# Kernel optimization log

Hardware: AMD Instinct MI355X
Metric: run time of the kernel (lower is better)

Reference implementation:

```python
import jax, jax.numpy as jnp
import numpy as np

B, T, D_IN, D_OUT, N_FILT, MAX_T = 4, 2048, 512, 512, 24, 2048


def _hankel_filters(max_t: int, k: int) -> np.ndarray:
    # Z_{ij} = 2 / ((i+j)^3 - (i+j)), 1-indexed; top-|eig| eigenvectors
    idx = np.arange(1, max_t + 1, dtype=np.float64)
    ij = idx[None, :] + idx[:, None]
    Z = 2.0 / (ij ** 3 - ij)
    w, v = np.linalg.eigh(Z)
    top = np.argsort(-np.abs(w))[:k]
    return v[:, top].astype(np.float32)  # (max_t, k)


def setup_inputs() -> dict:
    key = jax.random.key(0)
    kx, km = jax.random.split(key)
    x = jax.random.normal(kx, (B, T, D_IN), dtype=jnp.float32)
    filters = jnp.asarray(_hankel_filters(MAX_T, N_FILT))  # (MAX_T, N)
    # nn.Linear weight is (d_out, d_in); stacked -> (N, d_out, d_in)
    scale = 1.0 / np.sqrt(D_IN)
    M_weights = jax.random.uniform(km, (N_FILT, D_OUT, D_IN), dtype=jnp.float32,
                                   minval=-scale, maxval=scale)
    return {"x": x, "filters": filters, "M_weights": M_weights}


def reference(x, filters, M_weights):
    Tlen = x.shape[1]
    phi = filters[:Tlen]                       # (T, N)
    phi_e = phi[None, :, :, None]              # (1, T, N, 1)
    weighted = phi_e * x[:, :, None, :]        # (B, T, N, D_in)
    csum = jnp.cumsum(weighted, axis=1)        # causal cumulative projection
    # per-filter rectangular projection: (B,T,N,f) x (N,o,f) -> (B,T,N,o)
    modulated = jnp.einsum('btnf,nof->btno', csum, M_weights)
    return (phi_e * modulated).sum(axis=2)     # (B, T, D_out)
```

## Files before the change

kernel.cpp:

```cpp
#include <hip/hip_runtime.h>
#include <stdint.h>

#define BQ 4
#define TT 2048
#define DF 512
#define DOUT 512
#define NF 24
#define CHF 8

typedef __attribute__((ext_vector_type(8))) short short8;
typedef __attribute__((ext_vector_type(4))) float f32x4;

typedef __attribute__((address_space(3))) uint8_t       lds_u8;
typedef __attribute__((address_space(1))) const uint8_t glb_u8;

__device__ __forceinline__ float bf2f(unsigned short u) {
    union { unsigned int i; float f; } v; v.i = ((unsigned int)u) << 16; return v.f;
}
__device__ __forceinline__ unsigned short f2bf(float f) {
    union { float f; unsigned int i; } v; v.f = f;
    unsigned int r = v.i + 0x7FFFu + ((v.i >> 16) & 1u);
    return (unsigned short)(r >> 16);
}
__device__ __forceinline__ float lo16f(unsigned int u) { return __uint_as_float(u << 16); }
__device__ __forceinline__ float hi16f(unsigned int u) { return __uint_as_float(u & 0xffff0000u); }

__device__ __forceinline__ int plaus16(unsigned int h) {
    unsigned int e = (h >> 7) & 0xffu;
    return (e >= 97u && e <= 141u) || ((h & 0x7fffu) == 0u);
}

__global__ void k_detect(const unsigned int* __restrict__ X, int* __restrict__ flag)
{
    const int lane = threadIdx.x;
    int cnt = 0;
#pragma unroll
    for (int i = 0; i < 4; ++i) {
        unsigned int w = X[lane * 4 + i];
        cnt += (plaus16(w >> 16) && plaus16(w & 0xffffu)) ? 1 : 0;
    }
    for (int off = 32; off > 0; off >>= 1) cnt += __shfl_down(cnt, off);
    if (lane == 0) *flag = (cnt < 180) ? 1 : 0;
}

__global__ __launch_bounds__(256) void k_convert(
    const void* __restrict__ src, unsigned short* __restrict__ dst,
    const int* __restrict__ flag, int n4)
{
    const int isf32 = *flag;
    int i = blockIdx.x * 256 + threadIdx.x;
    const int stride = gridDim.x * 256;
    for (; i < n4; i += stride) {
        ushort4 o;
        if (isf32) {
            float4 v = ((const float4*)src)[i];
            o.x = f2bf(v.x); o.y = f2bf(v.y); o.z = f2bf(v.z); o.w = f2bf(v.w);
        } else {
            o = ((const ushort4*)src)[i];
        }
        ((ushort4*)dst)[i] = o;
    }
}

__global__ __launch_bounds__(256) void k_convf(
    const void* __restrict__ src, float* __restrict__ dst,
    const int* __restrict__ flag, int n)
{
    const int isf32 = *flag;
    int i = blockIdx.x * 256 + threadIdx.x;
    const int stride = gridDim.x * 256;
    for (; i < n; i += stride)
        dst[i] = isf32 ? ((const float*)src)[i]
                       : bf2f(((const unsigned short*)src)[i]);
}

__global__ __launch_bounds__(256, 3) void k_gemm_fast(
    const unsigned short* __restrict__ X,
    const unsigned short* __restrict__ Mw,
    const float* __restrict__ Fw,
    unsigned short* __restrict__ Z,
    float* __restrict__ Cs,
    int r0)
{
    __shared__ unsigned short sAB[128 * 136];
    __shared__ float sPhi[128];
    unsigned short* const sC = sAB;

    const int tid  = threadIdx.x;
    const int lane = tid & 63;
    const int w    = tid >> 6;
    const int wm   = w & 1, wn = w >> 1;
    const int tm   = blockIdx.x;
    const int on0  = blockIdx.y * 128;
    const int n    = blockIdx.z;

    const int rowg0 = r0 + tm * 128;
    if (tid < 128)
        sPhi[tid] = Fw[((rowg0 + tid) & (TT - 1)) * NF + n];

    const unsigned short* Ag = X + (size_t)rowg0 * DF;
    const unsigned short* Bg = Mw + (size_t)n * DOUT * DF + (size_t)on0 * DF;

    auto stage = [&](int kt, int buf) {
        const unsigned short* Ak = Ag + kt * 32;
        const unsigned short* Bk = Bg + kt * 32;
        lds_u8* base = (lds_u8*)sAB + buf * 16384;
#pragma unroll
        for (int i = 0; i < 2; ++i) {
            const int cbase = i * 256 + w * 64;
            const int c = cbase + lane;
            const int r = c >> 2, qs = c & 3;
            const int qg = qs ^ ((r >> 1) & 3);
            __builtin_amdgcn_global_load_lds(
                (const glb_u8*)(Ak + (size_t)r * DF + qg * 8),
                base + cbase * 16, 16, 0, 0);
            __builtin_amdgcn_global_load_lds(
                (const glb_u8*)(Bk + (size_t)r * DF + qg * 8),
                base + 8192 + cbase * 16, 16, 0, 0);
        }
    };

    f32x4 acc[4][4];
#pragma unroll
    for (int i = 0; i < 4; i++)
#pragma unroll
        for (int j = 0; j < 4; j++) acc[i][j] = (f32x4){0.f, 0.f, 0.f, 0.f};

    stage(0, 0);
    __syncthreads();

    const int lr = lane & 15;
    const int q  = lane >> 4;
    const int qsw = (q ^ ((lr >> 1) & 3)) * 8;

    for (int kt = 0; kt < DF / 32; ++kt) {
        const int cur = kt & 1;
        if (kt < DF / 32 - 1) stage(kt + 1, cur ^ 1);

        const unsigned short* sAc = sAB + cur * 8192;
        const unsigned short* sBc = sAc + 4096;
        short8 a[4], b[4];
#pragma unroll
        for (int i = 0; i < 4; i++)
            a[i] = *(const short8*)&sAc[(wm * 64 + i * 16 + lr) * 32 + qsw];
#pragma unroll
        for (int j = 0; j < 4; j++)
            b[j] = *(const short8*)&sBc[(wn * 64 + j * 16 + lr) * 32 + qsw];
#pragma unroll
        for (int i = 0; i < 4; i++)
#pragma unroll
            for (int j = 0; j < 4; j++)
                acc[i][j] = __builtin_amdgcn_mfma_f32_16x16x32_bf16(
                    a[i], b[j], acc[i][j], 0, 0, 0);

        __syncthreads();
    }

    const int rb = (lane >> 4) * 4;
#pragma unroll
    for (int i = 0; i < 4; i++)
#pragma unroll
        for (int j = 0; j < 4; j++)
#pragma unroll
            for (int r = 0; r < 4; r++) {
                int row = wm * 64 + i * 16 + rb + r;
                sC[row * 136 + wn * 64 + j * 16 + (lane & 15)] =
                    f2bf(acc[i][j][r] * sPhi[row]);
            }
    __syncthreads();

#pragma unroll
    for (int it = 0; it < 8; ++it) {
        int row = it * 16 + (tid >> 4);
        int col = (tid & 15) * 8;
        uint4 v = *(const uint4*)&sC[row * 136 + col];
        *(uint4*)&Z[((size_t)(tm * 128 + row) * NF + n) * 512 + on0 + col] = v;
    }

    {
        const int ci  = tid >> 4;
        const int col = (tid & 15) * 8;
        float s0=0.f,s1=0.f,s2=0.f,s3=0.f,s4=0.f,s5=0.f,s6=0.f,s7=0.f;
#pragma unroll
        for (int r = 0; r < CHF; ++r) {
            uint4 v = *(const uint4*)&sC[(ci * CHF + r) * 136 + col];
            s0 += lo16f(v.x); s1 += hi16f(v.x);
            s2 += lo16f(v.y); s3 += hi16f(v.y);
            s4 += lo16f(v.z); s5 += hi16f(v.z);
            s6 += lo16f(v.w); s7 += hi16f(v.w);
        }
        float* cp = &Cs[((size_t)(tm * 16 + ci) * NF + n) * 512 + on0 + col];
        *(float4*)cp       = make_float4(s0, s1, s2, s3);
        *(float4*)(cp + 4) = make_float4(s4, s5, s6, s7);
    }
}

__global__ __launch_bounds__(256, 2) void k_gemm(
    const void* __restrict__ Xv, const void* __restrict__ Mv,
    const void* __restrict__ Fv, const int* __restrict__ flag,
    unsigned short* __restrict__ Z, int r0, int o0, int W)
{
    __shared__ unsigned short sA[128 * 32];
    __shared__ unsigned short sB[128 * 32];
    __shared__ unsigned short sC[128 * 136];
    __shared__ float sPhi[128];

    const int isf32 = *flag;
    const int tid  = threadIdx.x;
    const int lane = tid & 63;
    const int w    = tid >> 6;
    const int wm   = w & 1, wn = w >> 1;
    const int tm   = blockIdx.x;
    const int on0  = o0 + blockIdx.y * 128;
    const int n    = blockIdx.z;

    const int rowg0 = r0 + tm * 128;
    if (tid < 128) {
        int t = (rowg0 + tid) & (TT - 1);
        sPhi[tid] = isf32 ? ((const float*)Fv)[t * NF + n]
                          : bf2f(((const unsigned short*)Fv)[t * NF + n]);
    }

    const unsigned short* Ah = (const unsigned short*)Xv + (size_t)rowg0 * DF;
    const unsigned short* Bh = (const unsigned short*)Mv +
        (size_t)n * DOUT * DF + (size_t)on0 * DF;
    const float* Af = (const float*)Xv + (size_t)rowg0 * DF;
    const float* Bf = (const float*)Mv + (size_t)n * DOUT * DF + (size_t)on0 * DF;

    f32x4 acc[4][4];
#pragma unroll
    for (int i = 0; i < 4; i++)
#pragma unroll
        for (int j = 0; j < 4; j++) acc[i][j] = (f32x4){0.f, 0.f, 0.f, 0.f};

    for (int kt = 0; kt < DF / 32; ++kt) {
        __syncthreads();
        if (!isf32) {
            const unsigned short* Ak = Ah + kt * 32;
            const unsigned short* Bk = Bh + kt * 32;
#pragma unroll
            for (int i = 0; i < 2; ++i) {
                const int c = i * 256 + tid;
                const int r = c >> 2, cc = (c & 3) * 8;
                *(short8*)&sA[r * 32 + cc] = *(const short8*)(Ak + (size_t)r * DF + cc);
                *(short8*)&sB[r * 32 + cc] = *(const short8*)(Bk + (size_t)r * DF + cc);
            }
        } else {
            const float* Ak = Af + kt * 32;
            const float* Bk = Bf + kt * 32;
#pragma unroll
            for (int i = 0; i < 2; ++i) {
                const int c = i * 256 + tid;
                const int r = c >> 2, cc = (c & 3) * 8;
                float4 a0 = *(const float4*)(Ak + (size_t)r * DF + cc);
                float4 a1 = *(const float4*)(Ak + (size_t)r * DF + cc + 4);
                float4 b0 = *(const float4*)(Bk + (size_t)r * DF + cc);
                float4 b1 = *(const float4*)(Bk + (size_t)r * DF + cc + 4);
                short8 sa, sb;
                sa[0]=(short)f2bf(a0.x); sa[1]=(short)f2bf(a0.y);
                sa[2]=(short)f2bf(a0.z); sa[3]=(short)f2bf(a0.w);
                sa[4]=(short)f2bf(a1.x); sa[5]=(short)f2bf(a1.y);
                sa[6]=(short)f2bf(a1.z); sa[7]=(short)f2bf(a1.w);
                sb[0]=(short)f2bf(b0.x); sb[1]=(short)f2bf(b0.y);
                sb[2]=(short)f2bf(b0.z); sb[3]=(short)f2bf(b0.w);
                sb[4]=(short)f2bf(b1.x); sb[5]=(short)f2bf(b1.y);
                sb[6]=(short)f2bf(b1.z); sb[7]=(short)f2bf(b1.w);
                *(short8*)&sA[r * 32 + cc] = sa;
                *(short8*)&sB[r * 32 + cc] = sb;
            }
        }
        __syncthreads();

        const int lr = lane & 15;
        const int lk = (lane >> 4) * 8;
        short8 a[4], b[4];
#pragma unroll
        for (int i = 0; i < 4; i++)
            a[i] = *(const short8*)&sA[(wm * 64 + i * 16 + lr) * 32 + lk];
#pragma unroll
        for (int j = 0; j < 4; j++)
            b[j] = *(const short8*)&sB[(wn * 64 + j * 16 + lr) * 32 + lk];
#pragma unroll
        for (int i = 0; i < 4; i++)
#pragma unroll
            for (int j = 0; j < 4; j++)
                acc[i][j] = __builtin_amdgcn_mfma_f32_16x16x32_bf16(
                    a[i], b[j], acc[i][j], 0, 0, 0);
    }

    const int rb = (lane >> 4) * 4;
#pragma unroll
    for (int i = 0; i < 4; i++)
#pragma unroll
        for (int j = 0; j < 4; j++)
#pragma unroll
            for (int r = 0; r < 4; r++) {
                int row = wm * 64 + i * 16 + rb + r;
                sC[row * 136 + wn * 64 + j * 16 + (lane & 15)] =
                    f2bf(acc[i][j][r] * sPhi[row]);
            }
    __syncthreads();
#pragma unroll
    for (int it = 0; it < 8; ++it) {
        int row = it * 16 + (tid >> 4);
        int col = (tid & 15) * 8;
        uint4 v = *(const uint4*)&sC[row * 136 + col];
        *(uint4*)&Z[((size_t)(tm * 128 + row) * NF + n) * W + (on0 - o0) + col] = v;
    }
}

__global__ __launch_bounds__(256, 2) void k_csum(
    const unsigned short* __restrict__ Z, float* __restrict__ Cs,
    int W, int CHs)
{
    const int c = blockIdx.x, n = blockIdx.y, tid = threadIdx.x;
    const unsigned short* p = Z + ((size_t)(c * CHs) * NF + n) * W + tid * 2;
    float sx = 0.f, sy = 0.f;
#pragma unroll 8
    for (int t = 0; t < CHs; ++t) {
        unsigned int u = *(const unsigned int*)(p + (size_t)t * NF * W);
        sx += lo16f(u);
        sy += hi16f(u);
    }
    float2* q = (float2*)&Cs[((size_t)c * NF + n) * W + tid * 2];
    *q = make_float2(sx, sy);
}

__global__ __launch_bounds__(256, 4) void k_prefix(
    float* __restrict__ Cs, float* __restrict__ Gc,
    int W, int rr, int nch, int nbat)
{
    const int tid  = threadIdx.x;
    const int lane = tid & 63;
    const int obw  = W >> 7;
    const int tasks = nbat * NF * obw;
    const int gw = blockIdx.x * 4 + (tid >> 6);
    if (gw >= tasks) return;
    const int perB = NF * obw;
    const int b    = gw / perB;
    const int rest = gw % perB;
    const int n    = rest / obw;
    const int ob   = rest % obw;
    const int opair = ob * 64 + lane;

    float* base = Cs + (size_t)b * nch * NF * W + (size_t)n * W + opair * 2;
    const size_t cstride = (size_t)NF * W;

    float cx = 0.f, cy = 0.f;
    if (nbat == 1 && rr != 0) {
        float2 g = *(const float2*)&Gc[(size_t)n * DOUT + opair * 2];
        cx = g.x; cy = g.y;
    }

    int c = 0;
    if (nch >= 16) {
        float2 v[8], w2[8];
#pragma unroll
        for (int k = 0; k < 8; ++k) v[k] = *(float2*)(base + (size_t)k * cstride);
        for (; c + 16 <= nch; c += 8) {
#pragma unroll
            for (int k = 0; k < 8; ++k)
                w2[k] = *(float2*)(base + (size_t)(c + 8 + k) * cstride);
#pragma unroll
            for (int k = 0; k < 8; ++k) {
                float2* p = (float2*)(base + (size_t)(c + k) * cstride);
                float2 t = v[k];
                *p = make_float2(cx, cy);
                cx += t.x; cy += t.y;
                v[k] = w2[k];
            }
        }
#pragma unroll
        for (int k = 0; k < 8; ++k) {
            float2* p = (float2*)(base + (size_t)(c + k) * cstride);
            float2 t = v[k];
            *p = make_float2(cx, cy);
            cx += t.x; cy += t.y;
        }
        c += 8;
    }
    for (; c < nch; ++c) {
        float2* p = (float2*)(base + (size_t)c * cstride);
        float2 t = *p;
        *p = make_float2(cx, cy);
        cx += t.x; cy += t.y;
    }

    if (nbat == 1)
        *(float2*)&Gc[(size_t)n * DOUT + opair * 2] = make_float2(cx, cy);
}

#define JLIST(F) F(0) F(1) F(2) F(3) F(4) F(5)

__global__ __launch_bounds__(256, 4) void k_scan(
    const unsigned short* __restrict__ Z, const float* __restrict__ Cs,
    const float* __restrict__ Fw, float* __restrict__ Out,
    int r0, int o0, int W, int CHs)
{
    __shared__ float sPhi[32 * NF];
    __shared__ float4 sP[4][8][64];
    const int cg = blockIdx.x, tid = threadIdx.x;
    const int g = tid >> 6, op = tid & 63;
    const int ng0 = g * 6;
    const int c4  = (blockIdx.y * 64 + op) * 4;
    const int act = (c4 + 4 <= W);
    const int c4u = act ? c4 : (W - 4);
    const int t0g = r0 + cg * CHs;
    const int t0 = t0g & (TT - 1);
    for (int i = tid; i < CHs * NF; i += 256)
        sPhi[i] = Fw[(t0 + i / NF) * NF + (i % NF)];
    __syncthreads();

#define DECLG(j) float gA##j, gB##j, gC##j, gD##j;
    JLIST(DECLG)
#define INITG(j) { float4 v = *(const float4*)&Cs[((size_t)cg * NF + ng0 + j) * W + c4u]; \
                   gA##j = v.x; gB##j = v.y; gC##j = v.z; gD##j = v.w; }
    JLIST(INITG)

    const unsigned short* zp = Z + ((size_t)cg * CHs * NF + ng0) * W + c4u;
    float* outb = Out + (size_t)t0g * DOUT + o0 + c4;
    for (int tb = 0; tb < CHs; tb += 8) {
#pragma unroll
        for (int tt = 0; tt < 8; ++tt) {
            float a0 = 0.f, a1 = 0.f, a2 = 0.f, a3 = 0.f;
            const float* php = &sPhi[(tb + tt) * NF + ng0];
#define UPDG(j) { uint2 u = *(const uint2*)(zp + (size_t)j * W); \
                  gA##j += lo16f(u.x); gB##j += hi16f(u.x); \
                  gC##j += lo16f(u.y); gD##j += hi16f(u.y); \
                  float ph = php[j]; \
                  a0 += ph * gA##j; a1 += ph * gB##j; \
                  a2 += ph * gC##j; a3 += ph * gD##j; }
            JLIST(UPDG)
            sP[g][tt][op] = make_float4(a0, a1, a2, a3);
            zp += (size_t)NF * W;
        }
        __syncthreads();
#pragma unroll
        for (int k = 0; k < 2; ++k) {
            const int tt = g * 2 + k;
            float4 p0 = sP[0][tt][op], p1 = sP[1][tt][op],
                   p2 = sP[2][tt][op], p3 = sP[3][tt][op];
            if (act)
                *(float4*)(outb + (size_t)(tb + tt) * DOUT) =
                    make_float4(p0.x + p1.x + p2.x + p3.x,
                                p0.y + p1.y + p2.y + p3.y,
                                p0.z + p1.z + p2.z + p3.z,
                                p0.w + p1.w + p2.w + p3.w);
        }
        __syncthreads();
    }
}

extern "C" void kernel_launch(void* const* d_in, const int* in_sizes, int n_in,
                              void* d_out, int out_size, void* d_ws, size_t ws_size,
                              hipStream_t stream)
{
    const void* X = d_in[0]; const void* Fil = d_in[1]; const void* Mw = d_in[2];
    for (int i = 0; i < n_in && i < 3; ++i) {
        if (in_sizes[i] == BQ * TT * DF)        X   = d_in[i];
        else if (in_sizes[i] == TT * NF)        Fil = d_in[i];
        else if (in_sizes[i] == NF * DOUT * DF) Mw  = d_in[i];
    }
    float* Out = (float*)d_out;

    const size_t offF = 256;
    const size_t nbF  = (size_t)TT * NF * 4;
    const size_t off0 = offF + nbF;
    const size_t nbX  = (size_t)BQ * TT * DF * 2;
    const size_t nbM  = (size_t)NF * DOUT * DF * 2;
    const size_t nbGc = (size_t)NF * DOUT * 4;

    int* flag = (int*)d_ws;
    float* Fw = (float*)((char*)d_ws + offF);

    hipLaunchKernelGGL(k_detect, dim3(1), dim3(64), 0, stream,
                       (const unsigned int*)X, flag);
    hipLaunchKernelGGL(k_convf, dim3(192), dim3(256), 0, stream,
                       Fil, Fw, flag, TT * NF);

    for (int G = BQ; G >= 2; G >>= 1) {
        const size_t zB  = (size_t)G * TT * NF * 512 * 2;
        const size_t csB = (size_t)(G * TT / CHF) * NF * 512 * 4;
        if (off0 + nbX + nbM + zB + csB > ws_size) continue;

        unsigned short* Xbf = (unsigned short*)((char*)d_ws + off0);
        unsigned short* Mbf = (unsigned short*)((char*)Xbf + nbX);
        unsigned short* Z   = (unsigned short*)((char*)Mbf + nbM);
        float* Cs = (float*)((char*)Z + zB);

        hipLaunchKernelGGL(k_convert, dim3(2048), dim3(256), 0, stream,
                           X, Xbf, flag, BQ * TT * DF / 4);
        hipLaunchKernelGGL(k_convert, dim3(3072), dim3(256), 0, stream,
                           Mw, Mbf, flag, NF * DOUT * DF / 4);

        const int nch = TT / CHF;
        for (int b0 = 0; b0 < BQ; b0 += G) {
            hipLaunchKernelGGL(k_gemm_fast, dim3(G * TT / 128, 4, NF), dim3(256),
                               0, stream, Xbf, Mbf, Fw, Z, Cs, b0 * TT);
            hipLaunchKernelGGL(k_prefix, dim3((G * NF * 4 + 3) / 4), dim3(256),
                               0, stream, Cs, (float*)nullptr, 512, 0, nch, G);
            hipLaunchKernelGGL(k_scan, dim3(G * nch, 2), dim3(256), 0, stream,
                               Z, Cs, Fw, Out, b0 * TT, 0, 512, CHF);
        }
        return;
    }

    {
        static const int rts[5] = {2048, 1024, 512, 256, 128};
        int RT = 0;
        for (int ri = 0; ri < 5; ++ri) {
            size_t need = off0 + nbX + nbM
                        + (size_t)rts[ri] * NF * 512 * 2
                        + (size_t)(rts[ri] / CHF) * NF * 512 * 4 + nbGc;
            if (need <= ws_size) { RT = rts[ri]; break; }
        }
        if (RT > 0) {
            unsigned short* Xbf = (unsigned short*)((char*)d_ws + off0);
            unsigned short* Mbf = (unsigned short*)((char*)Xbf + nbX);
            unsigned short* Z   = (unsigned short*)((char*)Mbf + nbM);
            float* Cs = (float*)((char*)Z + (size_t)RT * NF * 512 * 2);
            float* Gc = (float*)((char*)Cs + (size_t)(RT / CHF) * NF * 512 * 4);

            hipLaunchKernelGGL(k_convert, dim3(2048), dim3(256), 0, stream,
                               X, Xbf, flag, BQ * TT * DF / 4);
            hipLaunchKernelGGL(k_convert, dim3(3072), dim3(256), 0, stream,
                               Mw, Mbf, flag, NF * DOUT * DF / 4);

            const int nrr = TT / RT, nch = RT / CHF;
            for (int b = 0; b < BQ; ++b) {
                for (int rr = 0; rr < nrr; ++rr) {
                    const int r0 = b * TT + rr * RT;
                    hipLaunchKernelGGL(k_gemm_fast, dim3(RT / 128, 4, NF), dim3(256),
                                       0, stream, Xbf, Mbf, Fw, Z, Cs, r0);
                    hipLaunchKernelGGL(k_prefix, dim3((NF * 4 + 3) / 4), dim3(256),
                                       0, stream, Cs, Gc, 512, rr, nch, 1);
                    hipLaunchKernelGGL(k_scan, dim3(nch, 2), dim3(256), 0, stream,
                                       Z, Cs, Fw, Out, r0, 0, 512, CHF);
                }
            }
            return;
        }
    }

    static const int cRT[7] = {2048, 1024, 512, 256, 128, 128, 128};
    static const int cW[7]  = {512, 512, 512, 512, 512, 256, 128};
    int RTs = 128, W = 128;
    for (int ci = 0; ci < 7; ++ci) {
        size_t need = off0 + (size_t)cRT[ci] * NF * cW[ci] * 2
                    + (size_t)(cRT[ci] / 32) * NF * cW[ci] * 4 + nbGc;
        if (need <= ws_size) { RTs = cRT[ci]; W = cW[ci]; break; }
    }
    unsigned short* Z = (unsigned short*)((char*)d_ws + off0);
    float* Cs = (float*)((char*)Z + (size_t)RTs * NF * W * 2);
    float* Gc = (float*)((char*)Cs + (size_t)(RTs / 32) * NF * W * 4);

    const int nrr = TT / RTs, nch = RTs / 32;
    for (int b = 0; b < BQ; ++b) {
        for (int o0 = 0; o0 < DOUT; o0 += W) {
            for (int rr = 0; rr < nrr; ++rr) {
                const int r0 = b * TT + rr * RTs;
                hipLaunchKernelGGL(k_gemm, dim3(RTs / 128, W / 128, NF), dim3(256),
                                   0, stream, X, Mw, Fil, flag, Z, r0, o0, W);
                hipLaunchKernelGGL(k_csum, dim3(nch, NF), dim3(W / 2), 0, stream,
                                   Z, Cs, W, 32);
                hipLaunchKernelGGL(k_prefix, dim3((NF * (W / 128) + 3) / 4), dim3(256),
                                   0, stream, Cs, Gc, W, rr, nch, 1);
                hipLaunchKernelGGL(k_scan, dim3(nch, (W + 255) / 256), dim3(256),
                                   0, stream, Z, Cs, Fw, Out, r0, o0, W, 32);
            }
        }
    }
}
```

Baseline: 329.5 us.

## Fuse detect/convert prep kernels into one and swizzle GEMM workgroup order

Merges dtype detection, the X and M weight bf16 conversion, and the filter float conversion into a single k_prep kernel, replacing four launches with one on the main paths. Each block recomputes the detection flag locally in shared memory, which adds a small amount of redundant work per block. The GEMM kernel also remaps its linear workgroup id with an 8-way interleave when the grid is a multiple of 8, which changes how tiles are spread across XCDs and may affect cache locality. The fallback path still uses the old detect/convf launches.

```diff
diff --git a/kernel.cpp b/kernel.cpp
--- a/kernel.cpp
+++ b/kernel.cpp
@@ -43,25 +43,6 @@
     if (lane == 0) *flag = (cnt < 180) ? 1 : 0;
 }
 
-__global__ __launch_bounds__(256) void k_convert(
-    const void* __restrict__ src, unsigned short* __restrict__ dst,
-    const int* __restrict__ flag, int n4)
-{
-    const int isf32 = *flag;
-    int i = blockIdx.x * 256 + threadIdx.x;
-    const int stride = gridDim.x * 256;
-    for (; i < n4; i += stride) {
-        ushort4 o;
-        if (isf32) {
-            float4 v = ((const float4*)src)[i];
-            o.x = f2bf(v.x); o.y = f2bf(v.y); o.z = f2bf(v.z); o.w = f2bf(v.w);
-        } else {
-            o = ((const ushort4*)src)[i];
-        }
-        ((ushort4*)dst)[i] = o;
-    }
-}
-
 __global__ __launch_bounds__(256) void k_convf(
     const void* __restrict__ src, float* __restrict__ dst,
     const int* __restrict__ flag, int n)
@@ -72,6 +53,62 @@
     for (; i < n; i += stride)
         dst[i] = isf32 ? ((const float*)src)[i]
                        : bf2f(((const unsigned short*)src)[i]);
+}
+
+__global__ __launch_bounds__(256) void k_prep(
+    const void* __restrict__ X, const void* __restrict__ Mw,
+    const void* __restrict__ Fil,
+    unsigned short* __restrict__ Xbf, unsigned short* __restrict__ Mbf,
+    float* __restrict__ Fw, int n4x, int n4m, int n4f)
+{
+    __shared__ int sflag;
+    const int tid = threadIdx.x;
+    if (tid < 64) {
+        int cnt = 0;
+        const unsigned int* Xu = (const unsigned int*)X;
+#pragma unroll
+        for (int i = 0; i < 4; ++i) {
+            unsigned int wd = Xu[tid * 4 + i];
+            cnt += (plaus16(wd >> 16) && plaus16(wd & 0xffffu)) ? 1 : 0;
+        }
+        for (int off = 32; off > 0; off >>= 1) cnt += __shfl_down(cnt, off);
+        if (tid == 0) sflag = (cnt < 180) ? 1 : 0;
+    }
+    __syncthreads();
+    const int isf32 = sflag;
+
+    const int total = n4x + n4m + n4f;
+    for (int i = blockIdx.x * 256 + tid; i < total; i += gridDim.x * 256) {
+        if (i < n4x) {
+            ushort4 o;
+            if (isf32) {
+                float4 v = ((const float4*)X)[i];
+                o.x = f2bf(v.x); o.y = f2bf(v.y); o.z = f2bf(v.z); o.w = f2bf(v.w);
+            } else {
+                o = ((const ushort4*)X)[i];
+            }
+            ((ushort4*)Xbf)[i] = o;
+        } else if (i < n4x + n4m) {
+            const int j = i - n4x;
+            ushort4 o;
+            if (isf32) {
+                float4 v = ((const float4*)Mw)[j];
+                o.x = f2bf(v.x); o.y = f2bf(v.y); o.z = f2bf(v.z); o.w = f2bf(v.w);
+            } else {
+                o = ((const ushort4*)Mw)[j];
+            }
+            ((ushort4*)Mbf)[j] = o;
+        } else {
+            const int j = i - n4x - n4m;
+            if (isf32) {
+                ((float4*)Fw)[j] = ((const float4*)Fil)[j];
+            } else {
+                ushort4 u = ((const ushort4*)Fil)[j];
+                ((float4*)Fw)[j] = make_float4(bf2f(u.x), bf2f(u.y),
+                                               bf2f(u.z), bf2f(u.w));
+            }
+        }
+    }
 }
 
 __global__ __launch_bounds__(256, 3) void k_gemm_fast(
@@ -90,9 +127,16 @@
     const int lane = tid & 63;
     const int w    = tid >> 6;
     const int wm   = w & 1, wn = w >> 1;
-    const int tm   = blockIdx.x;
-    const int on0  = blockIdx.y * 128;
-    const int n    = blockIdx.z;
+
+    const int gx = gridDim.x, gy = gridDim.y;
+    const int nwg = gx * gy * gridDim.z;
+    int lid = blockIdx.x + gx * (blockIdx.y + gy * blockIdx.z);
+    int swz = lid;
+    if ((nwg & 7) == 0) swz = (lid & 7) * (nwg >> 3) + (lid >> 3);
+    const int tm   = swz % gx;
+    const int rest = swz / gx;
+    const int on0  = (rest % gy) * 128;
+    const int n    = rest / gy;
 
     const int rowg0 = r0 + tm * 128;
     if (tid < 128)
@@ -473,10 +517,9 @@
     int* flag = (int*)d_ws;
     float* Fw = (float*)((char*)d_ws + offF);
 
-    hipLaunchKernelGGL(k_detect, dim3(1), dim3(64), 0, stream,
-                       (const unsigned int*)X, flag);
-    hipLaunchKernelGGL(k_convf, dim3(192), dim3(256), 0, stream,
-                       Fil, Fw, flag, TT * NF);
+    const int n4x = BQ * TT * DF / 4;
+    const int n4m = NF * DOUT * DF / 4;
+    const int n4f = TT * NF / 4;
 
     for (int G = BQ; G >= 2; G >>= 1) {
         const size_t zB  = (size_t)G * TT * NF * 512 * 2;
@@ -488,10 +531,8 @@
         unsigned short* Z   = (unsigned short*)((char*)Mbf + nbM);
         float* Cs = (float*)((char*)Z + zB);
 
-        hipLaunchKernelGGL(k_convert, dim3(2048), dim3(256), 0, stream,
-                           X, Xbf, flag, BQ * TT * DF / 4);
-        hipLaunchKernelGGL(k_convert, dim3(3072), dim3(256), 0, stream,
-                           Mw, Mbf, flag, NF * DOUT * DF / 4);
+        hipLaunchKernelGGL(k_prep, dim3(2048), dim3(256), 0, stream,
+                           X, Mw, Fil, Xbf, Mbf, Fw, n4x, n4m, n4f);
 
         const int nch = TT / CHF;
         for (int b0 = 0; b0 < BQ; b0 += G) {
@@ -521,10 +562,8 @@
             float* Cs = (float*)((char*)Z + (size_t)RT * NF * 512 * 2);
             float* Gc = (float*)((char*)Cs + (size_t)(RT / CHF) * NF * 512 * 4);
 
-            hipLaunchKernelGGL(k_convert, dim3(2048), dim3(256), 0, stream,
-                               X, Xbf, flag, BQ * TT * DF / 4);
-            hipLaunchKernelGGL(k_convert, dim3(3072), dim3(256), 0, stream,
-                               Mw, Mbf, flag, NF * DOUT * DF / 4);
+            hipLaunchKernelGGL(k_prep, dim3(2048), dim3(256), 0, stream,
+                               X, Mw, Fil, Xbf, Mbf, Fw, n4x, n4m, n4f);
 
             const int nrr = TT / RT, nch = RT / CHF;
             for (int b = 0; b < BQ; ++b) {
@@ -541,6 +580,11 @@
             return;
         }
     }
+
+    hipLaunchKernelGGL(k_detect, dim3(1), dim3(64), 0, stream,
+                       (const unsigned int*)X, flag);
+    hipLaunchKernelGGL(k_convf, dim3(192), dim3(256), 0, stream,
+                       Fil, Fw, flag, TT * NF);
 
     static const int cRT[7] = {2048, 1024, 512, 256, 128, 128, 128};
     static const int cW[7]  = {512, 512, 512, 512, 512, 256, 128};
```

Result: no change. 333.5 us (+1.2%).
